# Performance work log

Hardware: AMD Instinct MI355X
Metric: run time of the kernel (lower is better)

The kernel has to match this reference:

```python
import jax, jax.numpy as jnp
import numpy as np

EPS = 1e-6
H, KV, D = 16, 4, 128  # num_heads, num_kv_heads, head_dim
ROPE_BASE = 1000000.0


def rmsnorm(x, w):
    # weight_offset = 1.0: scale is (w + 1)
    var = jnp.mean(x * x, axis=-1, keepdims=True)
    return x * jax.lax.rsqrt(var + EPS) * (w + 1.0)


def rope_tables(S, dtype):
    inv_freq = 1.0 / (ROPE_BASE ** (np.arange(0, D, 2, dtype=np.float32) / D))
    freqs = np.outer(np.arange(S, dtype=np.float32), inv_freq)  # [S, D/2]
    emb = np.concatenate([freqs, freqs], axis=-1)  # [S, D]
    return jnp.asarray(np.cos(emb), dtype), jnp.asarray(np.sin(emb), dtype)


def rotate_half(x):
    x1, x2 = jnp.split(x, 2, axis=-1)
    return jnp.concatenate([-x2, x1], axis=-1)


def setup_inputs() -> dict:
    key = jax.random.key(0)
    ks = jax.random.split(key, 5)
    B, S, HID = 2, 2048, 2048
    return {
        "x": jax.random.normal(ks[0], (B, S, HID), jnp.float32),
        "Wq": jax.random.normal(ks[1], (HID, 2 * H * D), jnp.float32) * 0.02,
        "Wk": jax.random.normal(ks[2], (HID, KV * D), jnp.float32) * 0.02,
        "Wv": jax.random.normal(ks[3], (HID, KV * D), jnp.float32) * 0.02,
        "Wo": jax.random.normal(ks[4], (H * D, HID), jnp.float32) * 0.02,
        "qn_w": jnp.zeros((D,), jnp.float32),
        "kn_w": jnp.zeros((D,), jnp.float32),
    }


def reference(x, Wq, Wk, Wv, Wo, qn_w, kn_w):
    B, S, _ = x.shape
    G = H // KV  # GQA group size
    # projections
    q_raw = (x @ Wq).reshape(B, S, H, 2 * D)
    q, gate = q_raw[..., :D], q_raw[..., D:]
    k = (x @ Wk).reshape(B, S, KV, D)
    v = (x @ Wv).reshape(B, S, KV, D)
    # QK RMSNorm (per head_dim)
    q = rmsnorm(q, qn_w)
    k = rmsnorm(k, kn_w)
    # RoPE (rotate-half form)
    cos, sin = rope_tables(S, x.dtype)  # [S, D]
    c = cos[None, :, None, :]
    s = sin[None, :, None, :]
    q = q * c + rotate_half(q) * s
    k = k * c + rotate_half(k) * s
    # grouped attention: avoid materializing repeated K/V
    # q: [B,S,H,D] -> [B,KV,G,S,D]; head h = kv*G + g matches repeat_interleave
    qg = q.transpose(0, 2, 1, 3).reshape(B, KV, G, S, D)
    kt = k.transpose(0, 2, 1, 3)  # [B,KV,S,D]
    vt = v.transpose(0, 2, 1, 3)  # [B,KV,S,D]
    scale = 1.0 / np.sqrt(D)
    scores = jnp.einsum("bkgsd,bktd->bkgst", qg, kt) * scale  # [B,KV,G,S,S]
    causal = jnp.tril(jnp.ones((S, S), bool))
    scores = jnp.where(causal, scores, jnp.finfo(scores.dtype).min)
    probs = jax.nn.softmax(scores, axis=-1)
    out = jnp.einsum("bkgst,bktd->bkgsd", probs, vt)  # [B,KV,G,S,D]
    out = out.reshape(B, H, S, D)
    # sigmoid gating from q projection
    gate = gate.transpose(0, 2, 1, 3)  # [B,H,S,D]
    out = out * jax.nn.sigmoid(gate)
    out = out.transpose(0, 2, 1, 3).reshape(B, S, H * D)
    return out @ Wo
```

## Files before the change

### kernel.cpp

```cpp
#include <hip/hip_runtime.h>
#include <hip/hip_bf16.h>

typedef unsigned short u16;
typedef __bf16 bf16x8 __attribute__((ext_vector_type(8)));
typedef float f32x4 __attribute__((ext_vector_type(4)));
typedef float f32x16 __attribute__((ext_vector_type(16)));

#define B_   2
#define S_   2048
#define HID_ 2048
#define H_   16
#define KV_  4
#define D_   128
#define TS_  5120

template <int V> struct ic { static constexpr int value = V; };

__device__ __forceinline__ u16 f2b(float f) {
  unsigned u = __float_as_uint(f);
  return (u16)((u + 0x7fffu + ((u >> 16) & 1u)) >> 16);
}
__device__ __forceinline__ float b2f(u16 h) {
  return __uint_as_float(((unsigned)h) << 16);
}
__device__ __forceinline__ unsigned pk2(float a, float b) {
  __hip_bfloat162 h = __float22bfloat162_rn(make_float2(a, b));
  unsigned u;
  __builtin_memcpy(&u, &h, 4);
  return u;
}
__device__ __forceinline__ void cstore(float* p, float v) { *p = v; }
__device__ __forceinline__ void cstore(u16* p, float v)   { *p = f2b(v); }

__device__ __forceinline__ void gl_lds16(const u16* g, u16* l) {
  __builtin_amdgcn_global_load_lds(
      (const __attribute__((address_space(1))) unsigned int*)g,
      (__attribute__((address_space(3))) unsigned int*)l, 16, 0, 0);
}


__global__ __launch_bounds__(256)
void cast_f2b_kernel(const float* __restrict__ in, u16* __restrict__ out) {
  const int idx = blockIdx.x * 256 + threadIdx.x;
  const int r = idx >> 8;
  const int k = (idx & 255) << 3;
  const float4 v0 = *(const float4*)(in + (size_t)r * 2048 + k);
  const float4 v1 = *(const float4*)(in + (size_t)r * 2048 + k + 4);
  uint4 w;
  w.x = pk2(v0.x, v0.y); w.y = pk2(v0.z, v0.w);
  w.z = pk2(v1.x, v1.y); w.w = pk2(v1.z, v1.w);
  const size_t off =
      ((((size_t)(r >> 4) * 64 + (k >> 5)) * 64) + ((k >> 3) & 3) * 16 +
       (r & 15)) * 8;
  *(uint4*)(out + off) = w;
}

__global__ __launch_bounds__(256)
void transpose_w_kernel(const float* __restrict__ in, u16* __restrict__ out,
                        int R, int Cc) {
  __shared__ u16 t[32][33];
  const int tx = threadIdx.x, ty = threadIdx.y;
  const int c0 = blockIdx.x * 32, r0 = blockIdx.y * 32;
#pragma unroll
  for (int i = 0; i < 4; i++)
    t[ty + i * 8][tx] = f2b(in[(size_t)(r0 + ty + i * 8) * Cc + c0 + tx]);
  __syncthreads();
  const int tid = ty * 32 + tx;
  if (tid < 128) {
    const int tl = tid >> 6, l = tid & 63, li = l & 15, quad = l >> 4;
    u16 vals[8];
#pragma unroll
    for (int e = 0; e < 8; e++) vals[e] = t[quad * 8 + e][tl * 16 + li];
    const size_t off =
        ((((size_t)(c0 >> 4) + tl) * (R >> 5) + (r0 >> 5)) * 64 + quad * 16 +
         li) * 8;
    *(uint4*)(out + off) = *(const uint4*)vals;
  }
}

__global__ __launch_bounds__(256)
void transpose_v_kernel(const u16* __restrict__ in, u16* __restrict__ out,
                        int tokstride) {
  __shared__ u16 t[32][33];
  const int tx = threadIdx.x, ty = threadIdx.y;
  const int jt = blockIdx.x, dt = blockIdx.y;
  const int s0 = jt * 32, d0 = dt * 32;
  const int z = blockIdx.z, b = z >> 2, kv = z & 3;
#pragma unroll
  for (int i = 0; i < 4; i++)
    t[ty + i * 8][tx] =
        in[(size_t)(b * S_ + s0 + ty + i * 8) * tokstride + kv * D_ + d0 + tx];
  __syncthreads();
  const int tid = ty * 32 + tx;
  if (tid < 128) {
    const int kk = tid >> 6, hi2 = (tid >> 5) & 1, d31 = tid & 31;
    u16 vals[8];
#pragma unroll
    for (int e = 0; e < 8; e++) vals[e] = t[kk * 16 + hi2 * 8 + e][d31];
    const size_t off =
        ((((size_t)(b * KV_ + kv) * 64 + jt) * 8 + dt * 2 + kk) * 64 +
         hi2 * 32 + d31) * 8;
    *(uint4*)(out + off) = *(const uint4*)vals;
  }
}

template <typename CT>
__global__ __launch_bounds__(256)
void gemm_nt(const u16* __restrict__ A, const u16* __restrict__ Bt,
             CT* __restrict__ C, int Md, int Nd, int Kd) {
  __shared__ u16 As[2][8 * 512];
  __shared__ u16 Bs[2][8 * 512];
  const int tid = threadIdx.x;
  const int lane = tid & 63;
  const int wave = tid >> 6;
  const int wm = wave >> 1, wn = wave & 1;
  const int li = lane & 15, quad = lane >> 4;

  const int id = blockIdx.x;
  const int grp = id & 7;
  const int r = id >> 3;
  const int px = Nd >> 10;
  const int m0 = (r & 31) * 128;
  const int n0 = (grp * px + (r >> 5)) * 128;

  f32x4 acc[4][4];
#pragma unroll
  for (int i = 0; i < 4; i++)
#pragma unroll
    for (int j = 0; j < 4; j++) acc[i][j] = (f32x4){0.f, 0.f, 0.f, 0.f};

  const size_t ts = (size_t)(Kd >> 5) * 512;
  const u16* Ab = A + ((size_t)(m0 >> 4) + wave * 2) * ts + lane * 8;
  const u16* Bb = Bt + ((size_t)(n0 >> 4) + wave * 2) * ts + lane * 8;

  auto stage = [&](int buf, int k0) {
    const size_t ko = (size_t)k0 * 16;
    gl_lds16(Ab + ko, &As[buf][(wave * 2) * 512]);
    gl_lds16(Ab + ts + ko, &As[buf][(wave * 2 + 1) * 512]);
    gl_lds16(Bb + ko, &Bs[buf][(wave * 2) * 512]);
    gl_lds16(Bb + ts + ko, &Bs[buf][(wave * 2 + 1) * 512]);
  };

  stage(0, 0);
  int cur = 0;
  for (int k0 = 0; k0 < Kd; k0 += 32) {
    __syncthreads();
    if (k0 + 32 < Kd) stage(cur ^ 1, k0 + 32);
    bf16x8 af[4], bfr[4];
#pragma unroll
    for (int mt = 0; mt < 4; mt++)
      af[mt] = *(const bf16x8*)&As[cur][(wm * 4 + mt) * 512 + lane * 8];
#pragma unroll
    for (int nt = 0; nt < 4; nt++)
      bfr[nt] = *(const bf16x8*)&Bs[cur][(wn * 4 + nt) * 512 + lane * 8];
#pragma unroll
    for (int mt = 0; mt < 4; mt++)
#pragma unroll
      for (int nt = 0; nt < 4; nt++)
        acc[mt][nt] = __builtin_amdgcn_mfma_f32_16x16x32_bf16(
            af[mt], bfr[nt], acc[mt][nt], 0, 0, 0);
    cur ^= 1;
  }
#pragma unroll
  for (int mt = 0; mt < 4; mt++) {
    const int row = m0 + wm * 64 + mt * 16 + quad * 4;
#pragma unroll
    for (int nt = 0; nt < 4; nt++) {
      const int col = n0 + wn * 64 + nt * 16 + li;
#pragma unroll
      for (int r2 = 0; r2 < 4; r2++)
        cstore(&C[(size_t)(row + r2) * Nd + col], acc[mt][nt][r2]);
    }
  }
}

__global__ __launch_bounds__(256)
void rmsrope_kernel(const u16* __restrict__ in, const float* __restrict__ w,
                    u16* __restrict__ out, int n_heads, int tok_stride,
                    int head_stride, float scale) {
  const int warp = (blockIdx.x << 2) + (threadIdx.x >> 6);
  const int lane = threadIdx.x & 63;
  const int h = warp % n_heads;
  const int tok = warp / n_heads;
  const int s = tok & (S_ - 1);
  const int b = tok >> 11;
  const u16* src = in + (size_t)tok * tok_stride + (size_t)h * head_stride;
  float x1 = b2f(src[lane]);
  float x2 = b2f(src[lane + 64]);
  float ss = x1 * x1 + x2 * x2;
#pragma unroll
  for (int off = 1; off < 64; off <<= 1) ss += __shfl_xor(ss, off);
  const float inv = rsqrtf(ss * (1.0f / 128.0f) + 1e-6f) * scale;
  x1 *= inv * (w[lane] + 1.0f);
  x2 *= inv * (w[lane + 64] + 1.0f);
  const float invf = exp2f((float)lane * (-19.931568569324174f / 64.0f));
  const float ang = (float)s * invf;
  float sn, c;
  sincosf(ang, &sn, &c);
  const int wq = lane >> 4, hi = (lane >> 3) & 1, e = lane & 7;
  const size_t tb = (((size_t)b * n_heads + h) * 64 + (s >> 5)) * 4096;
  const size_t o1 = tb + (size_t)(wq * 64 + hi * 32 + (s & 31)) * 8 + e;
  out[o1]        = f2b(x1 * c - x2 * sn);
  out[o1 + 2048] = f2b(x2 * c + x1 * sn);
}

__global__ __launch_bounds__(128, 2)
void attn_kernel(const u16* __restrict__ Q, const u16* __restrict__ Kr,
                 const u16* __restrict__ Vt, const u16* __restrict__ qraw,
                 u16* __restrict__ Ag) {
  __shared__ __align__(16) float Wscr[2][2176];
  __shared__ float Mdump[2][32], Ldump[2][32];

  const int tid = threadIdx.x;
  const int lane = tid & 63;
  const int wv = tid >> 6;
  const int l31 = lane & 31, hi = lane >> 5;

  const int id = blockIdx.x;
  const int grp = id & 7;
  const int b = grp >> 2, kv = grp & 3;
  const int rest = id >> 3;
  const int hh = rest & 3;
  const int t = 63 - (rest >> 2);
  const int h = (kv << 2) | hh;
  const int bh = (b << 4) | h;
  const int rs = t * 32;

  const u16* Qb = Q + ((size_t)bh * 64 + t) * 4096;
  const u16* Kb = Kr + (size_t)(b * KV_ + kv) * 64 * 4096;
  const u16* Vb = Vt + (size_t)(b * KV_ + kv) * 64 * 4096;

  bf16x8 qf[8];
#pragma unroll
  for (int w = 0; w < 8; w++)
    qf[w] = *(const bf16x8*)(Qb + w * 512 + lane * 8);

  float m_s = -1e30f, l_s = 0.f;
  f32x16 oacc[4];
#pragma unroll
  for (int dt = 0; dt < 4; dt++)
#pragma unroll
    for (int i = 0; i < 16; i++) oacc[dt][i] = 0.f;

  const int h0 = (t + 2) >> 1;
  const int klo = wv ? h0 : 0;
  const int khi = wv ? (t + 1) : h0;

  bf16x8 kf[8];
  auto loadK = [&](int jt) {
    const u16* kp = Kb + (size_t)jt * 4096 + lane * 8;
#pragma unroll
    for (int w = 0; w < 8; w++) kf[w] = *(const bf16x8*)(kp + w * 512);
  };

  auto step = [&](int jt) {
    const u16* vp = Vb + (size_t)jt * 4096 + lane * 8;
    bf16x8 vf[8];
#pragma unroll
    for (int f = 0; f < 8; f++)
      vf[f] = *(const bf16x8*)(vp + f * 512);

    f32x16 s0, s1;
#pragma unroll
    for (int i = 0; i < 16; i++) { s0[i] = 0.f; s1[i] = 0.f; }
#pragma unroll
    for (int dc = 0; dc < 4; dc++) {
      s0 = __builtin_amdgcn_mfma_f32_32x32x16_bf16(kf[2 * dc], qf[2 * dc], s0,
                                                   0, 0, 0);
      s1 = __builtin_amdgcn_mfma_f32_32x32x16_bf16(kf[2 * dc + 1],
                                                   qf[2 * dc + 1], s1, 0, 0, 0);
    }
    if (jt + 1 < khi) loadK(jt + 1);
    f32x16 s = s0 + s1;

    if (jt == t) {
#pragma unroll
      for (int r = 0; r < 16; r++) {
        const int kl = (r & 3) + 8 * (r >> 2) + 4 * hi;
        if (kl > l31) s[r] = -1e30f;
      }
    }
    float mx4[4];
#pragma unroll
    for (int g = 0; g < 4; g++)
      mx4[g] = fmaxf(fmaxf(s[4 * g], s[4 * g + 1]),
                     fmaxf(s[4 * g + 2], s[4 * g + 3]));
    float mx = fmaxf(fmaxf(mx4[0], mx4[1]), fmaxf(mx4[2], mx4[3]));
    mx = fmaxf(mx, __shfl_xor(mx, 32));
    const bool defer = __all(mx - m_s <= 8.f);
    const float mn = defer ? m_s : fmaxf(m_s, mx);
    if (!defer) {
      const float alpha = __expf(m_s - mn);
      m_s = mn;
      l_s *= alpha;
#pragma unroll
      for (int dt = 0; dt < 4; dt++)
#pragma unroll
        for (int i = 0; i < 16; i++) oacc[dt][i] *= alpha;
    }
    float rs4[4];
#pragma unroll
    for (int g = 0; g < 4; g++) {
      float e0 = __expf(s[4 * g + 0] - mn);
      float e1 = __expf(s[4 * g + 1] - mn);
      float e2 = __expf(s[4 * g + 2] - mn);
      float e3 = __expf(s[4 * g + 3] - mn);
      s[4 * g + 0] = e0; s[4 * g + 1] = e1;
      s[4 * g + 2] = e2; s[4 * g + 3] = e3;
      rs4[g] = (e0 + e1) + (e2 + e3);
    }
    float rsum = (rs4[0] + rs4[1]) + (rs4[2] + rs4[3]);
    rsum += __shfl_xor(rsum, 32);
    l_s += rsum;
    unsigned a0 = pk2(s[0], s[1]),  b0 = pk2(s[2], s[3]);
    unsigned c0 = pk2(s[4], s[5]),  d0 = pk2(s[6], s[7]);
    unsigned e0 = pk2(s[8], s[9]),  f0 = pk2(s[10], s[11]);
    unsigned g0 = pk2(s[12], s[13]), h0w = pk2(s[14], s[15]);
    unsigned r1 = __shfl_xor(hi ? a0 : c0, 32);
    unsigned r2 = __shfl_xor(hi ? b0 : d0, 32);
    unsigned r3 = __shfl_xor(hi ? e0 : g0, 32);
    unsigned r4 = __shfl_xor(hi ? f0 : h0w, 32);
    union U16B { unsigned u[4]; bf16x8 v; };
    U16B p0, p1;
    p0.u[0] = hi ? r1 : a0;  p0.u[1] = hi ? r2 : b0;
    p0.u[2] = hi ? c0 : r1;  p0.u[3] = hi ? d0 : r2;
    p1.u[0] = hi ? r3 : e0;  p1.u[1] = hi ? r4 : f0;
    p1.u[2] = hi ? g0 : r3;  p1.u[3] = hi ? h0w : r4;
#pragma unroll
    for (int dt = 0; dt < 4; dt++) {
      oacc[dt] = __builtin_amdgcn_mfma_f32_32x32x16_bf16(vf[dt * 2], p0.v,
                                                         oacc[dt], 0, 0, 0);
      oacc[dt] = __builtin_amdgcn_mfma_f32_32x32x16_bf16(vf[dt * 2 + 1], p1.v,
                                                         oacc[dt], 0, 0, 0);
    }
  };

  if (klo < khi) {
    loadK(klo);
    for (int jt = klo; jt < khi; jt++) step(jt);
  }

  float* myscr = &Wscr[wv][0];
  auto dumpO = [&](auto wvc) {
    constexpr int WV = decltype(wvc)::value;
#pragma unroll
    for (int i = 0; i < 2; i++) {
#pragma unroll
      for (int g = 0; g < 4; g++) {
        f32x4 w;
        w[0] = oacc[(1 - WV) * 2 + i][4 * g + 0];
        w[1] = oacc[(1 - WV) * 2 + i][4 * g + 1];
        w[2] = oacc[(1 - WV) * 2 + i][4 * g + 2];
        w[3] = oacc[(1 - WV) * 2 + i][4 * g + 3];
        *(f32x4*)&myscr[l31 * 68 + i * 32 + 8 * g + 4 * hi] = w;
      }
    }
    if (hi == 0) {
      Mdump[WV][l31] = m_s;
      Ldump[WV][l31] = l_s;
    }
  };
  if (wv == 0) dumpO(ic<0>{}); else dumpO(ic<1>{});
  __syncthreads();
  auto finO = [&](auto wvc) {
    constexpr int WV = decltype(wvc)::value;
    const float* oscr = &Wscr[1 - WV][0];
    const float mo = Mdump[1 - WV][l31];
    const float lo2 = Ldump[1 - WV][l31];
    const float mm = fmaxf(m_s, mo);
    const float as = __expf(m_s - mm), ao = __expf(mo - mm);
    const float linv = 1.f / (l_s * as + lo2 * ao);
    const size_t tok = (size_t)b * S_ + rs + l31;
    const u16* gp = qraw + tok * TS_ + h * 256 + 128;
#pragma unroll
    for (int i = 0; i < 2; i++) {
#pragma unroll
      for (int g = 0; g < 4; g++) {
        const int dbase = (WV * 2 + i) * 32 + 8 * g + 4 * hi;
        const int dg = h * 128 + dbase;
        f32x4 oo = *(const f32x4*)&oscr[l31 * 68 + i * 32 + 8 * g + 4 * hi];
        uint2 gv = *(const uint2*)(gp + dbase);
        float g0 = b2f((u16)(gv.x & 0xffff)), g1 = b2f((u16)(gv.x >> 16));
        float g2 = b2f((u16)(gv.y & 0xffff)), g3 = b2f((u16)(gv.y >> 16));
        float o0 = (oacc[WV * 2 + i][4 * g + 0] * as + oo[0] * ao) * linv /
                   (1.f + __expf(-g0));
        float o1 = (oacc[WV * 2 + i][4 * g + 1] * as + oo[1] * ao) * linv /
                   (1.f + __expf(-g1));
        float o2 = (oacc[WV * 2 + i][4 * g + 2] * as + oo[2] * ao) * linv /
                   (1.f + __expf(-g2));
        float o3 = (oacc[WV * 2 + i][4 * g + 3] * as + oo[3] * ao) * linv /
                   (1.f + __expf(-g3));
        const size_t off =
            (((tok >> 4) * 64 + (dg >> 5)) * 64 + ((dg >> 3) & 3) * 16 +
             (tok & 15)) * 8 + 4 * hi;
        *(uint2*)(Ag + off) = make_uint2(pk2(o0, o1), pk2(o2, o3));
      }
    }
  };
  if (wv == 0) finO(ic<0>{}); else finO(ic<1>{});
}

extern "C" void kernel_launch(void* const* d_in, const int* in_sizes, int n_in,
                              void* d_out, int out_size, void* d_ws,
                              size_t ws_size, hipStream_t stream) {
  const float* x  = (const float*)d_in[0];
  const float* Wq = (const float*)d_in[1];
  const float* Wk = (const float*)d_in[2];
  const float* Wv = (const float*)d_in[3];
  const float* Wo = (const float*)d_in[4];
  const float* qn = (const float*)d_in[5];
  const float* kn = (const float*)d_in[6];
  float* out = (float*)d_out;
  char* ws = (char*)d_ws;

  u16* xb    = (u16*)(ws + 0);
  u16* Wqt   = (u16*)(ws + 16777216);
  u16* Wkvt  = (u16*)(ws + 33554432);
  u16* Wot   = (u16*)(ws + 37748736);
  u16* qkraw = (u16*)(ws + 46137344);
  u16* Vtb   = (u16*)(ws + 88080384);
  u16* Kr    = (u16*)(ws + 92274688);
  u16* Ag    = (u16*)(ws + 96468992);
  u16* Qr = xb;

  cast_f2b_kernel<<<4096, 256, 0, stream>>>(x, xb);
  transpose_w_kernel<<<dim3(128, 64), dim3(32, 8), 0, stream>>>(Wq, Wqt, 2048, 4096);
  transpose_w_kernel<<<dim3(16, 64), dim3(32, 8), 0, stream>>>(Wk, Wkvt, 2048, 512);
  transpose_w_kernel<<<dim3(16, 64), dim3(32, 8), 0, stream>>>(Wv, Wkvt + 512 * 2048,
                                                               2048, 512);
  transpose_w_kernel<<<dim3(64, 64), dim3(32, 8), 0, stream>>>(Wo, Wot, 2048, 2048);

  gemm_nt<u16><<<1280, 256, 0, stream>>>(xb, Wqt, qkraw, 4096, TS_, 2048);

  rmsrope_kernel<<<16384, 256, 0, stream>>>(qkraw, qn, Qr, 16, TS_, 256,
                                            0.08838834764831845f);
  rmsrope_kernel<<<4096, 256, 0, stream>>>(qkraw + 4096, kn, Kr, 4, TS_, 128,
                                           1.0f);
  transpose_v_kernel<<<dim3(64, 4, 8), dim3(32, 8), 0, stream>>>(
      qkraw + 4096 + 512, Vtb, TS_);

  attn_kernel<<<2048, 128, 0, stream>>>(Qr, Kr, Vtb, qkraw, Ag);
  gemm_nt<float><<<512, 256, 0, stream>>>(Ag, Wot, out, 4096, 2048, 2048);
}
```

Measured before the change: 382.2 us.

## Merge prep kernels into two launches, remap GEMM tiles, raise MFMA priority

Folds the x cast and the four weight transposes into one launch, and the Q/K RMSNorm-RoPE and V transpose into a second, so the number of kernel launches and the tail gaps between them go down. The GEMM tile mapping now derives m0/n0 with division and modulo by px rather than fixed 31/5 masks, which changes the order in which blocks visit tiles. The attention kernel raises wave priority around its MFMA sequences so matrix work gets issued ahead of other waves. The merged kernels branch on the block index, which adds some divergence and shared-memory use to blocks that do not need it.

```diff
diff --git a/kernel.cpp b/kernel.cpp
--- a/kernel.cpp
+++ b/kernel.cpp
@@ -40,32 +40,42 @@
 
 
 __global__ __launch_bounds__(256)
-void cast_f2b_kernel(const float* __restrict__ in, u16* __restrict__ out) {
-  const int idx = blockIdx.x * 256 + threadIdx.x;
-  const int r = idx >> 8;
-  const int k = (idx & 255) << 3;
-  const float4 v0 = *(const float4*)(in + (size_t)r * 2048 + k);
-  const float4 v1 = *(const float4*)(in + (size_t)r * 2048 + k + 4);
-  uint4 w;
-  w.x = pk2(v0.x, v0.y); w.y = pk2(v0.z, v0.w);
-  w.z = pk2(v1.x, v1.y); w.w = pk2(v1.z, v1.w);
-  const size_t off =
-      ((((size_t)(r >> 4) * 64 + (k >> 5)) * 64) + ((k >> 3) & 3) * 16 +
-       (r & 15)) * 8;
-  *(uint4*)(out + off) = w;
-}
-
-__global__ __launch_bounds__(256)
-void transpose_w_kernel(const float* __restrict__ in, u16* __restrict__ out,
-                        int R, int Cc) {
+void prep0_kernel(const float* __restrict__ Wq, const float* __restrict__ Wk,
+                  const float* __restrict__ Wv, const float* __restrict__ Wo,
+                  const float* __restrict__ x, u16* __restrict__ Wqt,
+                  u16* __restrict__ Wkvt, u16* __restrict__ Wot,
+                  u16* __restrict__ xb) {
   __shared__ u16 t[32][33];
-  const int tx = threadIdx.x, ty = threadIdx.y;
-  const int c0 = blockIdx.x * 32, r0 = blockIdx.y * 32;
+  const int tid = threadIdx.x;
+  int idx = blockIdx.x;
+  if (idx >= 14336) {
+    idx -= 14336;
+    const int gi = idx * 256 + tid;
+    const int r = gi >> 8;
+    const int k = (gi & 255) << 3;
+    const float4 v0 = *(const float4*)(x + (size_t)r * 2048 + k);
+    const float4 v1 = *(const float4*)(x + (size_t)r * 2048 + k + 4);
+    uint4 w;
+    w.x = pk2(v0.x, v0.y); w.y = pk2(v0.z, v0.w);
+    w.z = pk2(v1.x, v1.y); w.w = pk2(v1.z, v1.w);
+    const size_t off =
+        ((((size_t)(r >> 4) * 64 + (k >> 5)) * 64) + ((k >> 3) & 3) * 16 +
+         (r & 15)) * 8;
+    *(uint4*)(xb + off) = w;
+    return;
+  }
+  const float* in; u16* out; int Cc, bx, by;
+  if (idx < 8192)       { in = Wq; out = Wqt; Cc = 4096; bx = idx & 127; by = idx >> 7; }
+  else if (idx < 9216)  { idx -= 8192; in = Wk; out = Wkvt; Cc = 512; bx = idx & 15; by = idx >> 4; }
+  else if (idx < 10240) { idx -= 9216; in = Wv; out = Wkvt + (size_t)512 * 2048; Cc = 512; bx = idx & 15; by = idx >> 4; }
+  else                  { idx -= 10240; in = Wo; out = Wot; Cc = 2048; bx = idx & 63; by = idx >> 6; }
+  const int R = 2048;
+  const int tx = tid & 31, ty = tid >> 5;
+  const int c0 = bx * 32, r0 = by * 32;
 #pragma unroll
   for (int i = 0; i < 4; i++)
     t[ty + i * 8][tx] = f2b(in[(size_t)(r0 + ty + i * 8) * Cc + c0 + tx]);
   __syncthreads();
-  const int tid = ty * 32 + tx;
   if (tid < 128) {
     const int tl = tid >> 6, l = tid & 63, li = l & 15, quad = l >> 4;
     u16 vals[8];
@@ -78,113 +88,17 @@
   }
 }
 
-__global__ __launch_bounds__(256)
-void transpose_v_kernel(const u16* __restrict__ in, u16* __restrict__ out,
-                        int tokstride) {
-  __shared__ u16 t[32][33];
-  const int tx = threadIdx.x, ty = threadIdx.y;
-  const int jt = blockIdx.x, dt = blockIdx.y;
-  const int s0 = jt * 32, d0 = dt * 32;
-  const int z = blockIdx.z, b = z >> 2, kv = z & 3;
-#pragma unroll
-  for (int i = 0; i < 4; i++)
-    t[ty + i * 8][tx] =
-        in[(size_t)(b * S_ + s0 + ty + i * 8) * tokstride + kv * D_ + d0 + tx];
-  __syncthreads();
-  const int tid = ty * 32 + tx;
-  if (tid < 128) {
-    const int kk = tid >> 6, hi2 = (tid >> 5) & 1, d31 = tid & 31;
-    u16 vals[8];
-#pragma unroll
-    for (int e = 0; e < 8; e++) vals[e] = t[kk * 16 + hi2 * 8 + e][d31];
-    const size_t off =
-        ((((size_t)(b * KV_ + kv) * 64 + jt) * 8 + dt * 2 + kk) * 64 +
-         hi2 * 32 + d31) * 8;
-    *(uint4*)(out + off) = *(const uint4*)vals;
-  }
-}
-
-template <typename CT>
-__global__ __launch_bounds__(256)
-void gemm_nt(const u16* __restrict__ A, const u16* __restrict__ Bt,
-             CT* __restrict__ C, int Md, int Nd, int Kd) {
-  __shared__ u16 As[2][8 * 512];
-  __shared__ u16 Bs[2][8 * 512];
-  const int tid = threadIdx.x;
+__device__ __forceinline__ void rmsrope_body(
+    int relblk, int tid, const u16* __restrict__ in,
+    const float* __restrict__ w, u16* __restrict__ out, int n_heads,
+    int head_stride, float scale) {
+  const int warp = (relblk << 2) + (tid >> 6);
   const int lane = tid & 63;
-  const int wave = tid >> 6;
-  const int wm = wave >> 1, wn = wave & 1;
-  const int li = lane & 15, quad = lane >> 4;
-
-  const int id = blockIdx.x;
-  const int grp = id & 7;
-  const int r = id >> 3;
-  const int px = Nd >> 10;
-  const int m0 = (r & 31) * 128;
-  const int n0 = (grp * px + (r >> 5)) * 128;
-
-  f32x4 acc[4][4];
-#pragma unroll
-  for (int i = 0; i < 4; i++)
-#pragma unroll
-    for (int j = 0; j < 4; j++) acc[i][j] = (f32x4){0.f, 0.f, 0.f, 0.f};
-
-  const size_t ts = (size_t)(Kd >> 5) * 512;
-  const u16* Ab = A + ((size_t)(m0 >> 4) + wave * 2) * ts + lane * 8;
-  const u16* Bb = Bt + ((size_t)(n0 >> 4) + wave * 2) * ts + lane * 8;
-
-  auto stage = [&](int buf, int k0) {
-    const size_t ko = (size_t)k0 * 16;
-    gl_lds16(Ab + ko, &As[buf][(wave * 2) * 512]);
-    gl_lds16(Ab + ts + ko, &As[buf][(wave * 2 + 1) * 512]);
-    gl_lds16(Bb + ko, &Bs[buf][(wave * 2) * 512]);
-    gl_lds16(Bb + ts + ko, &Bs[buf][(wave * 2 + 1) * 512]);
-  };
-
-  stage(0, 0);
-  int cur = 0;
-  for (int k0 = 0; k0 < Kd; k0 += 32) {
-    __syncthreads();
-    if (k0 + 32 < Kd) stage(cur ^ 1, k0 + 32);
-    bf16x8 af[4], bfr[4];
-#pragma unroll
-    for (int mt = 0; mt < 4; mt++)
-      af[mt] = *(const bf16x8*)&As[cur][(wm * 4 + mt) * 512 + lane * 8];
-#pragma unroll
-    for (int nt = 0; nt < 4; nt++)
-      bfr[nt] = *(const bf16x8*)&Bs[cur][(wn * 4 + nt) * 512 + lane * 8];
-#pragma unroll
-    for (int mt = 0; mt < 4; mt++)
-#pragma unroll
-      for (int nt = 0; nt < 4; nt++)
-        acc[mt][nt] = __builtin_amdgcn_mfma_f32_16x16x32_bf16(
-            af[mt], bfr[nt], acc[mt][nt], 0, 0, 0);
-    cur ^= 1;
-  }
-#pragma unroll
-  for (int mt = 0; mt < 4; mt++) {
-    const int row = m0 + wm * 64 + mt * 16 + quad * 4;
-#pragma unroll
-    for (int nt = 0; nt < 4; nt++) {
-      const int col = n0 + wn * 64 + nt * 16 + li;
-#pragma unroll
-      for (int r2 = 0; r2 < 4; r2++)
-        cstore(&C[(size_t)(row + r2) * Nd + col], acc[mt][nt][r2]);
-    }
-  }
-}
-
-__global__ __launch_bounds__(256)
-void rmsrope_kernel(const u16* __restrict__ in, const float* __restrict__ w,
-                    u16* __restrict__ out, int n_heads, int tok_stride,
-                    int head_stride, float scale) {
-  const int warp = (blockIdx.x << 2) + (threadIdx.x >> 6);
-  const int lane = threadIdx.x & 63;
   const int h = warp % n_heads;
   const int tok = warp / n_heads;
   const int s = tok & (S_ - 1);
   const int b = tok >> 11;
-  const u16* src = in + (size_t)tok * tok_stride + (size_t)h * head_stride;
+  const u16* src = in + (size_t)tok * TS_ + (size_t)h * head_stride;
   float x1 = b2f(src[lane]);
   float x2 = b2f(src[lane + 64]);
   float ss = x1 * x1 + x2 * x2;
@@ -204,6 +118,115 @@
   out[o1 + 2048] = f2b(x2 * c + x1 * sn);
 }
 
+__global__ __launch_bounds__(256)
+void prep1_kernel(const u16* __restrict__ qkraw, const float* __restrict__ qn,
+                  const float* __restrict__ kn, u16* __restrict__ Qr,
+                  u16* __restrict__ Kr, u16* __restrict__ Vtb) {
+  const int tid = threadIdx.x;
+  int blk = blockIdx.x;
+  if (blk < 16384) {
+    rmsrope_body(blk, tid, qkraw, qn, Qr, 16, 256, 0.08838834764831845f);
+    return;
+  }
+  blk -= 16384;
+  if (blk < 4096) {
+    rmsrope_body(blk, tid, qkraw + 4096, kn, Kr, 4, 128, 1.0f);
+    return;
+  }
+  blk -= 4096;
+  __shared__ u16 t[32][33];
+  const int tx = tid & 31, ty = tid >> 5;
+  const int jt = blk & 63, dt = (blk >> 6) & 3, z = blk >> 8;
+  const int s0 = jt * 32, d0 = dt * 32;
+  const int b = z >> 2, kv = z & 3;
+  const u16* in = qkraw + 4096 + 512;
+#pragma unroll
+  for (int i = 0; i < 4; i++)
+    t[ty + i * 8][tx] =
+        in[(size_t)(b * S_ + s0 + ty + i * 8) * TS_ + kv * D_ + d0 + tx];
+  __syncthreads();
+  if (tid < 128) {
+    const int kk = tid >> 6, hi2 = (tid >> 5) & 1, d31 = tid & 31;
+    u16 vals[8];
+#pragma unroll
+    for (int e = 0; e < 8; e++) vals[e] = t[kk * 16 + hi2 * 8 + e][d31];
+    const size_t off =
+        ((((size_t)(b * KV_ + kv) * 64 + jt) * 8 + dt * 2 + kk) * 64 +
+         hi2 * 32 + d31) * 8;
+    *(uint4*)(Vtb + off) = *(const uint4*)vals;
+  }
+}
+
+template <typename CT>
+__global__ __launch_bounds__(256)
+void gemm_nt(const u16* __restrict__ A, const u16* __restrict__ Bt,
+             CT* __restrict__ C, int Md, int Nd, int Kd) {
+  __shared__ u16 As[2][8 * 512];
+  __shared__ u16 Bs[2][8 * 512];
+  const int tid = threadIdx.x;
+  const int lane = tid & 63;
+  const int wave = tid >> 6;
+  const int wm = wave >> 1, wn = wave & 1;
+  const int li = lane & 15, quad = lane >> 4;
+
+  const int id = blockIdx.x;
+  const int grp = id & 7;
+  const int r = id >> 3;
+  const int px = Nd >> 10;
+  const int m0 = (r / px) * 128;
+  const int n0 = (grp * px + (r % px)) * 128;
+
+  f32x4 acc[4][4];
+#pragma unroll
+  for (int i = 0; i < 4; i++)
+#pragma unroll
+    for (int j = 0; j < 4; j++) acc[i][j] = (f32x4){0.f, 0.f, 0.f, 0.f};
+
+  const size_t ts = (size_t)(Kd >> 5) * 512;
+  const u16* Ab = A + ((size_t)(m0 >> 4) + wave * 2) * ts + lane * 8;
+  const u16* Bb = Bt + ((size_t)(n0 >> 4) + wave * 2) * ts + lane * 8;
+
+  auto stage = [&](int buf, int k0) {
+    const size_t ko = (size_t)k0 * 16;
+    gl_lds16(Ab + ko, &As[buf][(wave * 2) * 512]);
+    gl_lds16(Ab + ts + ko, &As[buf][(wave * 2 + 1) * 512]);
+    gl_lds16(Bb + ko, &Bs[buf][(wave * 2) * 512]);
+    gl_lds16(Bb + ts + ko, &Bs[buf][(wave * 2 + 1) * 512]);
+  };
+
+  stage(0, 0);
+  int cur = 0;
+  for (int k0 = 0; k0 < Kd; k0 += 32) {
+    __syncthreads();
+    if (k0 + 32 < Kd) stage(cur ^ 1, k0 + 32);
+    bf16x8 af[4], bfr[4];
+#pragma unroll
+    for (int mt = 0; mt < 4; mt++)
+      af[mt] = *(const bf16x8*)&As[cur][(wm * 4 + mt) * 512 + lane * 8];
+#pragma unroll
+    for (int nt = 0; nt < 4; nt++)
+      bfr[nt] = *(const bf16x8*)&Bs[cur][(wn * 4 + nt) * 512 + lane * 8];
+#pragma unroll
+    for (int mt = 0; mt < 4; mt++)
+#pragma unroll
+      for (int nt = 0; nt < 4; nt++)
+        acc[mt][nt] = __builtin_amdgcn_mfma_f32_16x16x32_bf16(
+            af[mt], bfr[nt], acc[mt][nt], 0, 0, 0);
+    cur ^= 1;
+  }
+#pragma unroll
+  for (int mt = 0; mt < 4; mt++) {
+    const int row = m0 + wm * 64 + mt * 16 + quad * 4;
+#pragma unroll
+    for (int nt = 0; nt < 4; nt++) {
+      const int col = n0 + wn * 64 + nt * 16 + li;
+#pragma unroll
+      for (int r2 = 0; r2 < 4; r2++)
+        cstore(&C[(size_t)(row + r2) * Nd + col], acc[mt][nt][r2]);
+    }
+  }
+}
+
 __global__ __launch_bounds__(128, 2)
 void attn_kernel(const u16* __restrict__ Q, const u16* __restrict__ Kr,
                  const u16* __restrict__ Vt, const u16* __restrict__ qraw,
@@ -263,6 +286,7 @@
     f32x16 s0, s1;
 #pragma unroll
     for (int i = 0; i < 16; i++) { s0[i] = 0.f; s1[i] = 0.f; }
+    __builtin_amdgcn_s_setprio(1);
 #pragma unroll
     for (int dc = 0; dc < 4; dc++) {
       s0 = __builtin_amdgcn_mfma_f32_32x32x16_bf16(kf[2 * dc], qf[2 * dc], s0,
@@ -270,6 +294,7 @@
       s1 = __builtin_amdgcn_mfma_f32_32x32x16_bf16(kf[2 * dc + 1],
                                                    qf[2 * dc + 1], s1, 0, 0, 0);
     }
+    __builtin_amdgcn_s_setprio(0);
     if (jt + 1 < khi) loadK(jt + 1);
     f32x16 s = s0 + s1;
 
@@ -326,6 +351,7 @@
     p0.u[2] = hi ? c0 : r1;  p0.u[3] = hi ? d0 : r2;
     p1.u[0] = hi ? r3 : e0;  p1.u[1] = hi ? r4 : f0;
     p1.u[2] = hi ? g0 : r3;  p1.u[3] = hi ? h0w : r4;
+    __builtin_amdgcn_s_setprio(1);
 #pragma unroll
     for (int dt = 0; dt < 4; dt++) {
       oacc[dt] = __builtin_amdgcn_mfma_f32_32x32x16_bf16(vf[dt * 2], p0.v,
@@ -333,6 +359,7 @@
       oacc[dt] = __builtin_amdgcn_mfma_f32_32x32x16_bf16(vf[dt * 2 + 1], p1.v,
                                                          oacc[dt], 0, 0, 0);
     }
+    __builtin_amdgcn_s_setprio(0);
   };
 
   if (klo < khi) {
@@ -423,21 +450,11 @@
   u16* Ag    = (u16*)(ws + 96468992);
   u16* Qr = xb;
 
-  cast_f2b_kernel<<<4096, 256, 0, stream>>>(x, xb);
-  transpose_w_kernel<<<dim3(128, 64), dim3(32, 8), 0, stream>>>(Wq, Wqt, 2048, 4096);
-  transpose_w_kernel<<<dim3(16, 64), dim3(32, 8), 0, stream>>>(Wk, Wkvt, 2048, 512);
-  transpose_w_kernel<<<dim3(16, 64), dim3(32, 8), 0, stream>>>(Wv, Wkvt + 512 * 2048,
-                                                               2048, 512);
-  transpose_w_kernel<<<dim3(64, 64), dim3(32, 8), 0, stream>>>(Wo, Wot, 2048, 2048);
+  prep0_kernel<<<18432, 256, 0, stream>>>(Wq, Wk, Wv, Wo, x, Wqt, Wkvt, Wot, xb);
 
   gemm_nt<u16><<<1280, 256, 0, stream>>>(xb, Wqt, qkraw, 4096, TS_, 2048);
 
-  rmsrope_kernel<<<16384, 256, 0, stream>>>(qkraw, qn, Qr, 16, TS_, 256,
-                                            0.08838834764831845f);
-  rmsrope_kernel<<<4096, 256, 0, stream>>>(qkraw + 4096, kn, Kr, 4, TS_, 128,
-                                           1.0f);
-  transpose_v_kernel<<<dim3(64, 4, 8), dim3(32, 8), 0, stream>>>(
-      qkraw + 4096 + 512, Vtb, TS_);
+  prep1_kernel<<<22528, 256, 0, stream>>>(qkraw, qn, kn, Qr, Kr, Vtb);
 
   attn_kernel<<<2048, 128, 0, stream>>>(Qr, Kr, Vtb, qkraw, Ag);
   gemm_nt<float><<<512, 256, 0, stream>>>(Ag, Wot, out, 4096, 2048, 2048);
```

Measured after the change: 363.4 us. 1.05x faster.
